# Optimization experiments

Measured on AMD Instinct MI355X. Metric: run time of the kernel, lower is better.

## Reference

```python
import jax, jax.numpy as jnp
import numpy as np

N, C, D, G, FC0, FC1, TOPK = 1024, 2, 1024, 16, 64, 16, 10
DG = D // G  # 64, per-group dim for WQ/WK
OPG = D // G  # 64, conv output channels per group (dim[2]=1024, groups=16)


def setup_inputs() -> dict:
    key = jax.random.key(0)
    ks = jax.random.split(key, 11)
    s = 0.02
    return {
        "f_a": jax.random.normal(ks[0], (N, C, D), jnp.float32),
        "position_embedding": jax.random.uniform(ks[1], (C, N, N, FC0), jnp.float32),
        "iou": jax.random.uniform(ks[2], (C, N, N), jnp.float32),
        "WG_w": jax.random.normal(ks[3], (FC1, FC0), jnp.float32) * s,
        "WG_b": jnp.zeros((FC1,), jnp.float32),
        "WK_w": jax.random.normal(ks[4], (D, D), jnp.float32) * s,
        "WK_b": jnp.zeros((D,), jnp.float32),
        "WQ_w": jax.random.normal(ks[5], (D, D), jnp.float32) * s,
        "WQ_b": jnp.zeros((D,), jnp.float32),
        "conv_w": jax.random.normal(ks[6], (D, D), jnp.float32) * s,  # [out=1024, in_per_group=1024] (1x1 kernel squeezed)
        "conv_b": jnp.zeros((D,), jnp.float32),
    }


def reference(f_a, position_embedding, iou, WG_w, WG_b, WK_w, WK_b, WQ_w, WQ_b, conv_w, conv_b):
    n = f_a.shape[0]
    k = min(n, TOPK)
    fa = jnp.transpose(f_a, (1, 0, 2))  # [C, N, D]

    # geometric bias: relu(Linear) -> [C, N, N, G] -> [C, G, N, N]
    w_g = jax.nn.relu(jnp.einsum('cmne,oe->cmno', position_embedding, WG_w) + WG_b)
    w_g = jnp.transpose(w_g, (0, 3, 1, 2))  # [C, G, N, N]

    # multi-head Q/K with per-group dim DG
    w_k = (jnp.einsum('cnd,ed->cne', fa, WK_w) + WK_b).reshape(C, n, G, DG)
    w_q = (jnp.einsum('cnd,ed->cne', fa, WQ_w) + WQ_b).reshape(C, n, G, DG)
    aff = jnp.einsum('cngd,cmgd->cgnm', w_q, w_k) / jnp.sqrt(jnp.float32(DG))  # [C, G, N, N]

    # iou_method == 'b': iou >= 1e-6 -> log(1)=0, else log(1e-6)
    log_iou = jnp.where(iou >= 1e-6, jnp.float32(0.0), jnp.log(jnp.float32(1e-6)))[:, None, :, :]

    w_mn = jnp.log(jnp.clip(w_g, 1e-6, None)) + aff + log_iou  # [C, G, N, N]

    # topk -> softmax over topk -> scatter back into dense [C, G, N, N]
    vals, idx = jax.lax.top_k(w_mn, k)
    soft = jax.nn.softmax(vals, axis=-1)
    ci = jnp.arange(C)[:, None, None, None]
    gi = jnp.arange(G)[None, :, None, None]
    ri = jnp.arange(n)[None, None, :, None]
    attn = jnp.zeros_like(w_mn).at[ci, gi, ri, idx].set(soft)

    # sparse attention-weighted aggregation of values
    out = jnp.einsum('cgnm,cmd->cgnd', attn, fa)  # [C, G, N, D]

    # grouped 1x1 conv: group g maps its D input channels to OPG output channels
    Wr = conv_w.reshape(G, OPG, D)  # [g, o_local, i]
    y = jnp.einsum('goi,cgni->ncgo', Wr, out).reshape(n, C, G * OPG) + conv_b  # [N, C, 1024]
    return y
```

## Files before the change

### kernel.cpp

```cpp
#include <hip/hip_runtime.h>
#include <math.h>

#define NT 1024
#define CD 2
#define DD 1024
#define GG 16
#define LOG1E6 -13.8155105579642740f
#define NEG_BIG -1e30f

typedef short bf16x8 __attribute__((ext_vector_type(8)));
typedef float f32x4  __attribute__((ext_vector_type(4)));

__device__ __forceinline__ unsigned short bf16_rne(float x) {
    unsigned int u = __float_as_uint(x);
    unsigned int r = (u + 0x7fffu + ((u >> 16) & 1u)) >> 16;
    return (unsigned short)r;
}

__device__ __forceinline__ void split3_8(const float* v, bf16x8& h, bf16x8& m, bf16x8& l) {
    #pragma unroll
    for (int e = 0; e < 8; ++e) {
        const float x = v[e];
        const unsigned short hb = bf16_rne(x);
        const float hf = __uint_as_float((unsigned int)hb << 16);
        const float r1 = x - hf;
        const unsigned short mb = bf16_rne(r1);
        const float mf = __uint_as_float((unsigned int)mb << 16);
        const float r2 = r1 - mf;
        const unsigned short lb = bf16_rne(r2);
        h[e] = (short)hb; m[e] = (short)mb; l[e] = (short)lb;
    }
}

__global__ __launch_bounds__(256) void k0_split(
    const float* __restrict__ fa, const float* __restrict__ Wq,
    const float* __restrict__ Wk, const float* __restrict__ Wc,
    unsigned short* __restrict__ Fh, unsigned short* __restrict__ Fm, unsigned short* __restrict__ Fl,
    unsigned short* __restrict__ WQh, unsigned short* __restrict__ WQm, unsigned short* __restrict__ WQl,
    unsigned short* __restrict__ WKh, unsigned short* __restrict__ WKm, unsigned short* __restrict__ WKl,
    unsigned short* __restrict__ WCh, unsigned short* __restrict__ WCm, unsigned short* __restrict__ WCl)
{
    const int reg = blockIdx.y;
    const float* src = (reg == 0) ? fa : (reg == 1) ? Wq : (reg == 2) ? Wk : Wc;
    unsigned short* dh = (reg == 0) ? Fh : (reg == 1) ? WQh : (reg == 2) ? WKh : WCh;
    unsigned short* dm = (reg == 0) ? Fm : (reg == 1) ? WQm : (reg == 2) ? WKm : WCm;
    unsigned short* dl = (reg == 0) ? Fl : (reg == 1) ? WQl : (reg == 2) ? WKl : WCl;
    const int nv = (reg == 0) ? (1 << 19) : (1 << 18);

    for (int v = blockIdx.x * 256 + threadIdx.x; v < nv; v += gridDim.x * 256) {
        float4 x4 = *(const float4*)&src[(size_t)v * 4];
        float xv[4] = {x4.x, x4.y, x4.z, x4.w};
        ushort4 h4, m4, l4;
        unsigned short hv[4], mv[4], lv[4];
        #pragma unroll
        for (int q = 0; q < 4; ++q) {
            const float x = xv[q];
            const unsigned short hb = bf16_rne(x);
            const float hf = __uint_as_float((unsigned int)hb << 16);
            const float r1 = x - hf;
            const unsigned short mb = bf16_rne(r1);
            const float mf = __uint_as_float((unsigned int)mb << 16);
            const unsigned short lb = bf16_rne(r1 - mf);
            hv[q] = hb; mv[q] = mb; lv[q] = lb;
        }
        h4.x = hv[0]; h4.y = hv[1]; h4.z = hv[2]; h4.w = hv[3];
        m4.x = mv[0]; m4.y = mv[1]; m4.z = mv[2]; m4.w = mv[3];
        l4.x = lv[0]; l4.y = lv[1]; l4.z = lv[2]; l4.w = lv[3];
        *(ushort4*)&dh[(size_t)v * 4] = h4;
        *(ushort4*)&dm[(size_t)v * 4] = m4;
        *(ushort4*)&dl[(size_t)v * 4] = l4;
    }
}

__global__ __launch_bounds__(256) void k1_mfma(
    const unsigned short* __restrict__ Fh, const unsigned short* __restrict__ Fm,
    const unsigned short* __restrict__ Fl,
    const unsigned short* __restrict__ WQh, const unsigned short* __restrict__ WQm,
    const unsigned short* __restrict__ WQl,
    const unsigned short* __restrict__ WKh, const unsigned short* __restrict__ WKm,
    const unsigned short* __restrict__ WKl,
    const unsigned short* __restrict__ WCh, const unsigned short* __restrict__ WCm,
    const unsigned short* __restrict__ WCl,
    const float* __restrict__ bq, const float* __restrict__ bk, const float* __restrict__ bc,
    float* __restrict__ Vo,
    unsigned short* __restrict__ QSh, unsigned short* __restrict__ QSm, unsigned short* __restrict__ QSl,
    unsigned short* __restrict__ KSh, unsigned short* __restrict__ KSm, unsigned short* __restrict__ KSl)
{
    const int et = blockIdx.x, rt = blockIdx.y, z = blockIdx.z;
    const unsigned short* Wh = (z == 0) ? WQh : (z == 1) ? WKh : WCh;
    const unsigned short* Wm = (z == 0) ? WQm : (z == 1) ? WKm : WCm;
    const unsigned short* Wl = (z == 0) ? WQl : (z == 1) ? WKl : WCl;
    const float* bb = (z == 0) ? bq : (z == 1) ? bk : bc;
    unsigned short* Sh = (z == 0) ? QSh : KSh;
    unsigned short* Sm = (z == 0) ? QSm : KSm;
    unsigned short* Sl = (z == 0) ? QSl : KSl;

    const int c  = rt >> 3;
    const int n0 = (rt & 7) * 128;
    const int r0 = rt * 128;
    const int e0 = et * 64;

    __shared__ unsigned short Ah[128][36], Am[128][36], Al[128][36];
    __shared__ unsigned short Bh[64][36],  Bm[64][36],  Bl[64][36];

    const int t    = threadIdx.x;
    const int wave = t >> 6, lane = t & 63;
    const int wr   = wave >> 1, wc = wave & 1;
    const int lrow = lane & 15, lk = lane >> 4;

    f32x4 acc[4][2];
    #pragma unroll
    for (int m = 0; m < 4; ++m)
        #pragma unroll
        for (int n = 0; n < 2; ++n) acc[m][n] = (f32x4){0.f, 0.f, 0.f, 0.f};

    for (int kt = 0; kt < 32; ++kt) {
        const int kb = kt * 32;
        #pragma unroll
        for (int p = 0; p < 2; ++p) {
            const int task = t + p * 256;
            const int row = task >> 2, seg = task & 3;
            const size_t gs = ((size_t)((n0 + row) * CD + c)) * DD + kb + seg * 8;
            *(uint4*)&Ah[row][seg * 8] = *(const uint4*)&Fh[gs];
            *(uint4*)&Am[row][seg * 8] = *(const uint4*)&Fm[gs];
            *(uint4*)&Al[row][seg * 8] = *(const uint4*)&Fl[gs];
        }
        {
            const int row = t >> 2, seg = t & 3;
            const size_t gs = ((size_t)(e0 + row)) * DD + kb + seg * 8;
            *(uint4*)&Bh[row][seg * 8] = *(const uint4*)&Wh[gs];
            *(uint4*)&Bm[row][seg * 8] = *(const uint4*)&Wm[gs];
            *(uint4*)&Bl[row][seg * 8] = *(const uint4*)&Wl[gs];
        }
        __syncthreads();
        {
            bf16x8 ah[4], am[4], al[4], bh[2], bm[2], bl[2];
            #pragma unroll
            for (int m = 0; m < 4; ++m) {
                const int row = wr * 64 + m * 16 + lrow;
                ah[m] = *(const bf16x8*)&Ah[row][lk * 8];
                am[m] = *(const bf16x8*)&Am[row][lk * 8];
                al[m] = *(const bf16x8*)&Al[row][lk * 8];
            }
            #pragma unroll
            for (int n = 0; n < 2; ++n) {
                const int row = wc * 32 + n * 16 + lrow;
                bh[n] = *(const bf16x8*)&Bh[row][lk * 8];
                bm[n] = *(const bf16x8*)&Bm[row][lk * 8];
                bl[n] = *(const bf16x8*)&Bl[row][lk * 8];
            }
            #pragma unroll
            for (int m = 0; m < 4; ++m)
                #pragma unroll
                for (int n = 0; n < 2; ++n) {
                    acc[m][n] = __builtin_amdgcn_mfma_f32_16x16x32_bf16(al[m], bh[n], acc[m][n], 0, 0, 0);
                    acc[m][n] = __builtin_amdgcn_mfma_f32_16x16x32_bf16(ah[m], bl[n], acc[m][n], 0, 0, 0);
                    acc[m][n] = __builtin_amdgcn_mfma_f32_16x16x32_bf16(am[m], bm[n], acc[m][n], 0, 0, 0);
                    acc[m][n] = __builtin_amdgcn_mfma_f32_16x16x32_bf16(am[m], bh[n], acc[m][n], 0, 0, 0);
                    acc[m][n] = __builtin_amdgcn_mfma_f32_16x16x32_bf16(ah[m], bm[n], acc[m][n], 0, 0, 0);
                    acc[m][n] = __builtin_amdgcn_mfma_f32_16x16x32_bf16(ah[m], bh[n], acc[m][n], 0, 0, 0);
                }
        }
        __syncthreads();
    }
    #pragma unroll
    for (int n = 0; n < 2; ++n) {
        const int e = e0 + wc * 32 + n * 16 + lrow;
        const float bias = bb[e];
        #pragma unroll
        for (int m = 0; m < 4; ++m) {
            const int r = r0 + wr * 64 + m * 16 + lk * 4;
            #pragma unroll
            for (int q = 0; q < 4; ++q) {
                const float val = acc[m][n][q] + bias;
                const size_t idx = ((size_t)(r + q)) * DD + e;
                if (z == 2) {
                    Vo[idx] = val;
                } else {
                    const unsigned short hb = bf16_rne(val);
                    const float hf = __uint_as_float((unsigned int)hb << 16);
                    const float r1 = val - hf;
                    const unsigned short mb = bf16_rne(r1);
                    const float mf = __uint_as_float((unsigned int)mb << 16);
                    const unsigned short lb = bf16_rne(r1 - mf);
                    Sh[idx] = hb; Sm[idx] = mb; Sl[idx] = lb;
                }
            }
        }
    }
}

__global__ __launch_bounds__(256) void k2a_mfma(
    const unsigned short* __restrict__ QSh, const unsigned short* __restrict__ QSm,
    const unsigned short* __restrict__ QSl,
    const unsigned short* __restrict__ KSh, const unsigned short* __restrict__ KSm,
    const unsigned short* __restrict__ KSl,
    float* __restrict__ aff)
{
    const int jt = blockIdx.x, it = blockIdx.y, cg = blockIdx.z;
    const int c = cg >> 4, g = cg & 15;
    const int i0 = it * 64, j0 = jt * 64;

    __shared__ unsigned short Qh[64][36], Qm[64][36], Ql[64][36];
    __shared__ unsigned short Kh[64][36], Km[64][36], Kl[64][36];

    const int t    = threadIdx.x;
    const int wave = t >> 6, lane = t & 63;
    const int wr   = wave >> 1, wc = wave & 1;
    const int lrow = lane & 15, lk = lane >> 4;

    f32x4 acc[2][2];
    #pragma unroll
    for (int m = 0; m < 2; ++m)
        #pragma unroll
        for (int n = 0; n < 2; ++n) acc[m][n] = (f32x4){0.f, 0.f, 0.f, 0.f};

    for (int kt = 0; kt < 2; ++kt) {
        const int kb = g * 64 + kt * 32;
        {
            const int row = t >> 2, seg = t & 3;
            const size_t qs = ((size_t)(c * NT + i0 + row)) * DD + kb + seg * 8;
            *(uint4*)&Qh[row][seg * 8] = *(const uint4*)&QSh[qs];
            *(uint4*)&Qm[row][seg * 8] = *(const uint4*)&QSm[qs];
            *(uint4*)&Ql[row][seg * 8] = *(const uint4*)&QSl[qs];
            const size_t ks = ((size_t)(c * NT + j0 + row)) * DD + kb + seg * 8;
            *(uint4*)&Kh[row][seg * 8] = *(const uint4*)&KSh[ks];
            *(uint4*)&Km[row][seg * 8] = *(const uint4*)&KSm[ks];
            *(uint4*)&Kl[row][seg * 8] = *(const uint4*)&KSl[ks];
        }
        __syncthreads();
        {
            bf16x8 qh[2], qm[2], ql[2], kh[2], km[2], kl[2];
            #pragma unroll
            for (int m = 0; m < 2; ++m) {
                const int row = wr * 32 + m * 16 + lrow;
                qh[m] = *(const bf16x8*)&Qh[row][lk * 8];
                qm[m] = *(const bf16x8*)&Qm[row][lk * 8];
                ql[m] = *(const bf16x8*)&Ql[row][lk * 8];
            }
            #pragma unroll
            for (int n = 0; n < 2; ++n) {
                const int row = wc * 32 + n * 16 + lrow;
                kh[n] = *(const bf16x8*)&Kh[row][lk * 8];
                km[n] = *(const bf16x8*)&Km[row][lk * 8];
                kl[n] = *(const bf16x8*)&Kl[row][lk * 8];
            }
            #pragma unroll
            for (int m = 0; m < 2; ++m)
                #pragma unroll
                for (int n = 0; n < 2; ++n) {
                    acc[m][n] = __builtin_amdgcn_mfma_f32_16x16x32_bf16(ql[m], kh[n], acc[m][n], 0, 0, 0);
                    acc[m][n] = __builtin_amdgcn_mfma_f32_16x16x32_bf16(qh[m], kl[n], acc[m][n], 0, 0, 0);
                    acc[m][n] = __builtin_amdgcn_mfma_f32_16x16x32_bf16(qm[m], km[n], acc[m][n], 0, 0, 0);
                    acc[m][n] = __builtin_amdgcn_mfma_f32_16x16x32_bf16(qm[m], kh[n], acc[m][n], 0, 0, 0);
                    acc[m][n] = __builtin_amdgcn_mfma_f32_16x16x32_bf16(qh[m], km[n], acc[m][n], 0, 0, 0);
                    acc[m][n] = __builtin_amdgcn_mfma_f32_16x16x32_bf16(qh[m], kh[n], acc[m][n], 0, 0, 0);
                }
        }
        __syncthreads();
    }
    #pragma unroll
    for (int m = 0; m < 2; ++m) {
        const int i = i0 + wr * 32 + m * 16 + lk * 4;
        #pragma unroll
        for (int n = 0; n < 2; ++n) {
            const int j = j0 + wc * 32 + n * 16 + lrow;
            #pragma unroll
            for (int q = 0; q < 4; ++q)
                aff[((size_t)cg * NT + i + q) * NT + j] = acc[m][n][q] * 0.125f;
        }
    }
}

__global__ __launch_bounds__(256, 4) void k3_scan(
    const float* __restrict__ pe, const float* __restrict__ iou,
    const float* __restrict__ WGw, const float* __restrict__ WGb,
    const float* __restrict__ aff,
    float* __restrict__ cv, int* __restrict__ ci)
{
    const int ch = blockIdx.x;
    const int it = blockIdx.y;
    const int c  = blockIdx.z;
    const int i0 = it * 8;

    __shared__ float wgl[8][16][33];
    __shared__ float ios[8][33];

    const int t = threadIdx.x;
    const int wave = t >> 6, lane = t & 63;
    const int lg = lane & 15, lk = lane >> 4;
    const int p_i = t >> 5, jq = t & 31;
    const int s_i = t >> 5, s_g = (t >> 1) & 15, s_h = t & 1;

    bf16x8 bh[2], bm[2], bl[2];
    #pragma unroll
    for (int kp = 0; kp < 2; ++kp) {
        float w8[8];
        float4 w0 = *(const float4*)&WGw[lg * 64 + kp * 32 + lk * 8];
        float4 w1 = *(const float4*)&WGw[lg * 64 + kp * 32 + lk * 8 + 4];
        w8[0]=w0.x; w8[1]=w0.y; w8[2]=w0.z; w8[3]=w0.w;
        w8[4]=w1.x; w8[5]=w1.y; w8[6]=w1.z; w8[7]=w1.w;
        split3_8(w8, bh[kp], bm[kp], bl[kp]);
    }
    const float bias = WGb[lg];

    float tv[10]; int tidx[10];
    #pragma unroll
    for (int q = 0; q < 10; ++q) { tv[q] = NEG_BIG; tidx[q] = 0; }

    for (int s = 0; s < 8; ++s) {
        const int j0 = ch * 256 + s * 32;
        {
            const float ia = iou[((size_t)c * NT + (i0 + p_i)) * NT + j0 + jq];
            ios[p_i][jq] = (ia >= 1e-6f) ? 0.f : LOG1E6;
        }
        #pragma unroll 1
        for (int rtt = 0; rtt < 4; ++rtt) {
            const int rt = wave * 4 + rtt;
            const int ib = rt >> 1;
            const int jb = (rt & 1) * 16;
            const float* pr = &pe[(((size_t)c * NT + (i0 + ib)) * NT + (j0 + jb + lg)) * 64];
            f32x4 acc = {0.f, 0.f, 0.f, 0.f};
            #pragma unroll
            for (int kp = 0; kp < 2; ++kp) {
                float a8[8];
                float4 v0 = *(const float4*)&pr[kp * 32 + lk * 8];
                float4 v1 = *(const float4*)&pr[kp * 32 + lk * 8 + 4];
                a8[0]=v0.x; a8[1]=v0.y; a8[2]=v0.z; a8[3]=v0.w;
                a8[4]=v1.x; a8[5]=v1.y; a8[6]=v1.z; a8[7]=v1.w;
                bf16x8 ah, am, al;
                split3_8(a8, ah, am, al);
                acc = __builtin_amdgcn_mfma_f32_16x16x32_bf16(al, bh[kp], acc, 0, 0, 0);
                acc = __builtin_amdgcn_mfma_f32_16x16x32_bf16(ah, bl[kp], acc, 0, 0, 0);
                acc = __builtin_amdgcn_mfma_f32_16x16x32_bf16(am, bm[kp], acc, 0, 0, 0);
                acc = __builtin_amdgcn_mfma_f32_16x16x32_bf16(am, bh[kp], acc, 0, 0, 0);
                acc = __builtin_amdgcn_mfma_f32_16x16x32_bf16(ah, bm[kp], acc, 0, 0, 0);
                acc = __builtin_amdgcn_mfma_f32_16x16x32_bf16(ah, bh[kp], acc, 0, 0, 0);
            }
            #pragma unroll
            for (int q = 0; q < 4; ++q) {
                const float v = acc[q] + bias;
                wgl[ib][lg][jb + lk * 4 + q] = (v > 1e-6f) ? __logf(v) : LOG1E6;
            }
        }
        __syncthreads();
        {
            const float* ar = &aff[(((size_t)(c * GG + s_g)) * NT + (i0 + s_i)) * NT + j0 + s_h * 16];
            const float* wl = &wgl[s_i][s_g][s_h * 16];
            const float* il = &ios[s_i][s_h * 16];
            #pragma unroll
            for (int j4 = 0; j4 < 16; j4 += 4) {
                float4 a4 = *(const float4*)&ar[j4];
                float av[4] = {a4.x, a4.y, a4.z, a4.w};
                #pragma unroll
                for (int q = 0; q < 4; ++q) {
                    const float val = wl[j4 + q] + av[q] + il[j4 + q];
                    if (val > tv[0]) {
                        const int ix = j0 + s_h * 16 + j4 + q;
                        #pragma unroll
                        for (int sl = 0; sl < 10; ++sl) {
                            const bool up   = (sl < 9) ? (val > tv[sl + 1]) : false;
                            const bool here = (val > tv[sl]);
                            const float ntv = up ? tv[sl + 1] : (here ? val : tv[sl]);
                            const int   nti = up ? tidx[sl + 1] : (here ? ix : tidx[sl]);
                            tv[sl] = ntv; tidx[sl] = nti;
                        }
                    }
                }
            }
        }
        __syncthreads();
    }

    float* mv = &wgl[0][0][0];
    int*   mi = (int*)(mv + 1280);
    const int pair = t >> 1;
    if (s_h == 1) {
        #pragma unroll
        for (int q = 0; q < 10; ++q) { mv[pair * 10 + q] = tv[q]; mi[pair * 10 + q] = tidx[q]; }
    }
    __syncthreads();
    if (s_h == 0) {
        for (int q = 9; q >= 0; --q) {
            const float val = mv[pair * 10 + q];
            const int   ix  = mi[pair * 10 + q];
            if (val > tv[0]) {
                #pragma unroll
                for (int sl = 0; sl < 10; ++sl) {
                    const bool up   = (sl < 9) ? (val > tv[sl + 1]) : false;
                    const bool here = (val > tv[sl]);
                    const float ntv = up ? tv[sl + 1] : (here ? val : tv[sl]);
                    const int   nti = up ? tidx[sl + 1] : (here ? ix : tidx[sl]);
                    tv[sl] = ntv; tidx[sl] = nti;
                }
            }
        }
        const size_t base = ((((size_t)c * NT + (i0 + s_i)) * GG + s_g) * 4 + ch) * 10;
        #pragma unroll
        for (int q = 0; q < 10; ++q) { cv[base + q] = tv[q]; ci[base + q] = tidx[q]; }
    }
}

__global__ __launch_bounds__(256) void k2b2_fin(
    const float* __restrict__ cv, const int* __restrict__ ci,
    const float* __restrict__ V, float* __restrict__ y)
{
    const int w    = (blockIdx.x << 2) + (threadIdx.x >> 6);
    const int lane = threadIdx.x & 63;
    const int c = w >> 14;
    const int i = (w >> 4) & (NT - 1);
    const int g = w & 15;

    float tv[10]; int tidx[10];
    #pragma unroll
    for (int q = 0; q < 10; ++q) { tv[q] = NEG_BIG; tidx[q] = 0; }

    const size_t base = (size_t)w * 40;
    for (int chn = 0; chn < 4; ++chn) {
        const float* cvp = &cv[base + chn * 10];
        const int*   cip = &ci[base + chn * 10];
        for (int q = 9; q >= 0; --q) {
            const float val = cvp[q];
            const int   ix  = cip[q];
            if (val > tv[0]) {
                #pragma unroll
                for (int sl = 0; sl < 10; ++sl) {
                    const bool up   = (sl < 9) ? (val > tv[sl + 1]) : false;
                    const bool here = (val > tv[sl]);
                    const float ntv = up ? tv[sl + 1] : (here ? val : tv[sl]);
                    const int   nti = up ? tidx[sl + 1] : (here ? ix : tidx[sl]);
                    tv[sl] = ntv; tidx[sl] = nti;
                }
            }
        }
    }
    const float m = tv[9];
    float wgt[10]; float sm = 0.f;
    #pragma unroll
    for (int q = 0; q < 10; ++q) { wgt[q] = __expf(tv[q] - m); sm += wgt[q]; }
    const float inv = 1.f / sm;
    float o = 0.f;
    #pragma unroll
    for (int q = 0; q < 10; ++q)
        o += (wgt[q] * inv) * V[((size_t)(c * NT + tidx[q])) * DD + g * 64 + lane];
    y[((size_t)i * CD + c) * DD + g * 64 + lane] = o;
}

extern "C" void kernel_launch(void* const* d_in, const int* in_sizes, int n_in,
                              void* d_out, int out_size, void* d_ws, size_t ws_size,
                              hipStream_t stream) {
    (void)in_sizes; (void)n_in; (void)out_size; (void)ws_size;
    const float* f_a = (const float*)d_in[0];
    const float* pe  = (const float*)d_in[1];
    const float* iou = (const float*)d_in[2];
    const float* WGw = (const float*)d_in[3];
    const float* WGb = (const float*)d_in[4];
    const float* WKw = (const float*)d_in[5];
    const float* WKb = (const float*)d_in[6];
    const float* WQw = (const float*)d_in[7];
    const float* WQb = (const float*)d_in[8];
    const float* Cw  = (const float*)d_in[9];
    const float* Cb  = (const float*)d_in[10];
    float* yout = (float*)d_out;

    float* ws  = (float*)d_ws;
    float* V   = ws + (2u << 21);
    float* aff = ws + (3u << 21);
    float* cv  = ws;
    int*   ci  = (int*)(ws + (1u << 21));
    unsigned short* sp = (unsigned short*)(ws + (3u << 21) + (1u << 25));
    const size_t FN = (size_t)CD * NT * DD;
    const size_t WN = (size_t)DD * DD;
    unsigned short* Fh  = sp;
    unsigned short* Fm  = Fh + FN;
    unsigned short* Fl  = Fm + FN;
    unsigned short* WQh = Fl + FN;
    unsigned short* WQm = WQh + WN;
    unsigned short* WQl = WQm + WN;
    unsigned short* WKh = WQl + WN;
    unsigned short* WKm = WKh + WN;
    unsigned short* WKl = WKm + WN;
    unsigned short* WCh = WKl + WN;
    unsigned short* WCm = WCh + WN;
    unsigned short* WCl = WCm + WN;
    unsigned short* QSh = WCl + WN;
    unsigned short* QSm = QSh + FN;
    unsigned short* QSl = QSm + FN;
    unsigned short* KSh = QSl + FN;
    unsigned short* KSm = KSh + FN;
    unsigned short* KSl = KSm + FN;

    k0_split<<<dim3(512, 4), 256, 0, stream>>>(f_a, WQw, WKw, Cw,
        Fh, Fm, Fl, WQh, WQm, WQl, WKh, WKm, WKl, WCh, WCm, WCl);
    k1_mfma<<<dim3(16, 16, 3), 256, 0, stream>>>(
        Fh, Fm, Fl, WQh, WQm, WQl, WKh, WKm, WKl, WCh, WCm, WCl,
        WQb, WKb, Cb, V, QSh, QSm, QSl, KSh, KSm, KSl);
    k2a_mfma<<<dim3(16, 16, 32), 256, 0, stream>>>(QSh, QSm, QSl, KSh, KSm, KSl, aff);
    k3_scan<<<dim3(4, 128, 2), 256, 0, stream>>>(pe, iou, WGw, WGb, aff, cv, ci);
    k2b2_fin<<<8192, 256, 0, stream>>>(cv, ci, V, yout);
}
```

Measured before the change: 410.5 us.

## Restructure top-k scan to one row per wave with shuffle merge

Each wave of the scan kernel now owns one query row. It consumes the MFMA accumulator layout directly to combine the geometric log-bias, the affinity and the IoU mask in registers, with no staging through shared memory. The two block-wide barriers per 32-column step and the shared-memory pair merge are replaced by a two-step cross-lane shuffle merge that also breaks ties by lower index. The grid doubles in rows and the occupancy hint rises to 5. The trade-off is lane-strided float4 reads of the affinity and IoU rows and heavier per-lane register use for the two top-10 lists.

```diff
diff --git a/kernel.cpp b/kernel.cpp
--- a/kernel.cpp
+++ b/kernel.cpp
@@ -272,25 +272,17 @@
     }
 }
 
-__global__ __launch_bounds__(256, 4) void k3_scan(
+__global__ __launch_bounds__(256, 5) void k3_scan(
     const float* __restrict__ pe, const float* __restrict__ iou,
     const float* __restrict__ WGw, const float* __restrict__ WGb,
     const float* __restrict__ aff,
     float* __restrict__ cv, int* __restrict__ ci)
 {
     const int ch = blockIdx.x;
-    const int it = blockIdx.y;
     const int c  = blockIdx.z;
-    const int i0 = it * 8;
-
-    __shared__ float wgl[8][16][33];
-    __shared__ float ios[8][33];
-
-    const int t = threadIdx.x;
-    const int wave = t >> 6, lane = t & 63;
+    const int wave = threadIdx.x >> 6, lane = threadIdx.x & 63;
+    const int i  = blockIdx.y * 4 + wave;
     const int lg = lane & 15, lk = lane >> 4;
-    const int p_i = t >> 5, jq = t & 31;
-    const int s_i = t >> 5, s_g = (t >> 1) & 15, s_h = t & 1;
 
     bf16x8 bh[2], bm[2], bl[2];
     #pragma unroll
@@ -308,83 +300,42 @@
     #pragma unroll
     for (int q = 0; q < 10; ++q) { tv[q] = NEG_BIG; tidx[q] = 0; }
 
-    for (int s = 0; s < 8; ++s) {
-        const int j0 = ch * 256 + s * 32;
-        {
-            const float ia = iou[((size_t)c * NT + (i0 + p_i)) * NT + j0 + jq];
-            ios[p_i][jq] = (ia >= 1e-6f) ? 0.f : LOG1E6;
-        }
-        #pragma unroll 1
-        for (int rtt = 0; rtt < 4; ++rtt) {
-            const int rt = wave * 4 + rtt;
-            const int ib = rt >> 1;
-            const int jb = (rt & 1) * 16;
-            const float* pr = &pe[(((size_t)c * NT + (i0 + ib)) * NT + (j0 + jb + lg)) * 64];
-            f32x4 acc = {0.f, 0.f, 0.f, 0.f};
-            #pragma unroll
-            for (int kp = 0; kp < 2; ++kp) {
-                float a8[8];
-                float4 v0 = *(const float4*)&pr[kp * 32 + lk * 8];
-                float4 v1 = *(const float4*)&pr[kp * 32 + lk * 8 + 4];
-                a8[0]=v0.x; a8[1]=v0.y; a8[2]=v0.z; a8[3]=v0.w;
-                a8[4]=v1.x; a8[5]=v1.y; a8[6]=v1.z; a8[7]=v1.w;
-                bf16x8 ah, am, al;
-                split3_8(a8, ah, am, al);
-                acc = __builtin_amdgcn_mfma_f32_16x16x32_bf16(al, bh[kp], acc, 0, 0, 0);
-                acc = __builtin_amdgcn_mfma_f32_16x16x32_bf16(ah, bl[kp], acc, 0, 0, 0);
-                acc = __builtin_amdgcn_mfma_f32_16x16x32_bf16(am, bm[kp], acc, 0, 0, 0);
-                acc = __builtin_amdgcn_mfma_f32_16x16x32_bf16(am, bh[kp], acc, 0, 0, 0);
-                acc = __builtin_amdgcn_mfma_f32_16x16x32_bf16(ah, bm[kp], acc, 0, 0, 0);
-                acc = __builtin_amdgcn_mfma_f32_16x16x32_bf16(ah, bh[kp], acc, 0, 0, 0);
-            }
-            #pragma unroll
-            for (int q = 0; q < 4; ++q) {
-                const float v = acc[q] + bias;
-                wgl[ib][lg][jb + lk * 4 + q] = (v > 1e-6f) ? __logf(v) : LOG1E6;
-            }
-        }
-        __syncthreads();
-        {
-            const float* ar = &aff[(((size_t)(c * GG + s_g)) * NT + (i0 + s_i)) * NT + j0 + s_h * 16];
-            const float* wl = &wgl[s_i][s_g][s_h * 16];
-            const float* il = &ios[s_i][s_h * 16];
-            #pragma unroll
-            for (int j4 = 0; j4 < 16; j4 += 4) {
-                float4 a4 = *(const float4*)&ar[j4];
-                float av[4] = {a4.x, a4.y, a4.z, a4.w};
-                #pragma unroll
-                for (int q = 0; q < 4; ++q) {
-                    const float val = wl[j4 + q] + av[q] + il[j4 + q];
-                    if (val > tv[0]) {
-                        const int ix = j0 + s_h * 16 + j4 + q;
-                        #pragma unroll
-                        for (int sl = 0; sl < 10; ++sl) {
-                            const bool up   = (sl < 9) ? (val > tv[sl + 1]) : false;
-                            const bool here = (val > tv[sl]);
-                            const float ntv = up ? tv[sl + 1] : (here ? val : tv[sl]);
-                            const int   nti = up ? tidx[sl + 1] : (here ? ix : tidx[sl]);
-                            tv[sl] = ntv; tidx[sl] = nti;
-                        }
-                    }
-                }
-            }
-        }
-        __syncthreads();
-    }
-
-    float* mv = &wgl[0][0][0];
-    int*   mi = (int*)(mv + 1280);
-    const int pair = t >> 1;
-    if (s_h == 1) {
-        #pragma unroll
-        for (int q = 0; q < 10; ++q) { mv[pair * 10 + q] = tv[q]; mi[pair * 10 + q] = tidx[q]; }
-    }
-    __syncthreads();
-    if (s_h == 0) {
-        for (int q = 9; q >= 0; --q) {
-            const float val = mv[pair * 10 + q];
-            const int   ix  = mi[pair * 10 + q];
+    const float* pebase = &pe[((size_t)c * NT + i) * NT * 64];
+    const float* afrow  = &aff[(((size_t)(c * GG + lg)) * NT + i) * NT];
+    const float* iorow  = &iou[((size_t)c * NT + i) * NT];
+
+    #pragma unroll 1
+    for (int tile = 0; tile < 16; ++tile) {
+        const int jb = ch * 256 + tile * 16;
+        const float* pr = &pebase[(size_t)(jb + lg) * 64];
+        f32x4 acc = {0.f, 0.f, 0.f, 0.f};
+        #pragma unroll
+        for (int kp = 0; kp < 2; ++kp) {
+            float a8[8];
+            float4 v0 = *(const float4*)&pr[kp * 32 + lk * 8];
+            float4 v1 = *(const float4*)&pr[kp * 32 + lk * 8 + 4];
+            a8[0]=v0.x; a8[1]=v0.y; a8[2]=v0.z; a8[3]=v0.w;
+            a8[4]=v1.x; a8[5]=v1.y; a8[6]=v1.z; a8[7]=v1.w;
+            bf16x8 ah, am, al;
+            split3_8(a8, ah, am, al);
+            acc = __builtin_amdgcn_mfma_f32_16x16x32_bf16(al, bh[kp], acc, 0, 0, 0);
+            acc = __builtin_amdgcn_mfma_f32_16x16x32_bf16(ah, bl[kp], acc, 0, 0, 0);
+            acc = __builtin_amdgcn_mfma_f32_16x16x32_bf16(am, bm[kp], acc, 0, 0, 0);
+            acc = __builtin_amdgcn_mfma_f32_16x16x32_bf16(am, bh[kp], acc, 0, 0, 0);
+            acc = __builtin_amdgcn_mfma_f32_16x16x32_bf16(ah, bm[kp], acc, 0, 0, 0);
+            acc = __builtin_amdgcn_mfma_f32_16x16x32_bf16(ah, bh[kp], acc, 0, 0, 0);
+        }
+        float4 a4 = *(const float4*)&afrow[jb + lk * 4];
+        float4 o4 = *(const float4*)&iorow[jb + lk * 4];
+        float av[4] = {a4.x, a4.y, a4.z, a4.w};
+        float ov[4] = {o4.x, o4.y, o4.z, o4.w};
+        #pragma unroll
+        for (int q = 0; q < 4; ++q) {
+            const float wg = acc[q] + bias;
+            const float lgv = (wg > 1e-6f) ? __logf(wg) : LOG1E6;
+            const float val = lgv + av[q] + ((ov[q] >= 1e-6f) ? 0.f : LOG1E6);
             if (val > tv[0]) {
+                const int ix = jb + lk * 4 + q;
                 #pragma unroll
                 for (int sl = 0; sl < 10; ++sl) {
                     const bool up   = (sl < 9) ? (val > tv[sl + 1]) : false;
@@ -395,7 +346,36 @@
                 }
             }
         }
-        const size_t base = ((((size_t)c * NT + (i0 + s_i)) * GG + s_g) * 4 + ch) * 10;
+    }
+
+    #pragma unroll
+    for (int step = 0; step < 2; ++step) {
+        const int ofs = (step == 0) ? 32 : 16;
+        float otv[10]; int oti[10];
+        #pragma unroll
+        for (int q = 0; q < 10; ++q) {
+            otv[q] = __shfl(tv[q], lane + ofs);
+            oti[q] = __shfl(tidx[q], lane + ofs);
+        }
+        #pragma unroll
+        for (int q = 9; q >= 0; --q) {
+            const float ov = otv[q]; const int oi = oti[q];
+            const bool g0 = (ov > tv[0]) || (ov == tv[0] && oi < tidx[0]);
+            if (g0) {
+                #pragma unroll
+                for (int sl = 0; sl < 10; ++sl) {
+                    const bool up   = (sl < 9) ? ((ov > tv[sl + 1]) || (ov == tv[sl + 1] && oi < tidx[sl + 1])) : false;
+                    const bool here = (ov > tv[sl]) || (ov == tv[sl] && oi < tidx[sl]);
+                    const float ntv = up ? tv[sl + 1] : (here ? ov : tv[sl]);
+                    const int   nti = up ? tidx[sl + 1] : (here ? oi : tidx[sl]);
+                    tv[sl] = ntv; tidx[sl] = nti;
+                }
+            }
+        }
+    }
+
+    if (lane < 16) {
+        const size_t base = ((((size_t)c * NT + i) * GG + lane) * 4 + ch) * 10;
         #pragma unroll
         for (int q = 0; q < 10; ++q) { cv[base + q] = tv[q]; ci[base + q] = tidx[q]; }
     }
@@ -496,6 +476,6 @@
         Fh, Fm, Fl, WQh, WQm, WQl, WKh, WKm, WKl, WCh, WCm, WCl,
         WQb, WKb, Cb, V, QSh, QSm, QSl, KSh, KSm, KSl);
     k2a_mfma<<<dim3(16, 16, 32), 256, 0, stream>>>(QSh, QSm, QSl, KSh, KSm, KSl, aff);
-    k3_scan<<<dim3(4, 128, 2), 256, 0, stream>>>(pe, iou, WGw, WGb, aff, cv, ci);
+    k3_scan<<<dim3(4, 256, 2), 256, 0, stream>>>(pe, iou, WGw, WGb, aff, cv, ci);
     k2b2_fin<<<8192, 256, 0, stream>>>(cv, ci, V, yout);
 }
```

New measurement: 438.4 us. +6.8%, slower.
